# Optimization experiments

Hardware: AMD Instinct MI355X
Metric: run time of the kernel (lower is better)

The kernel has to match this reference:

```python
import jax, jax.numpy as jnp
import numpy as np

N_ENT = 2000
GAT_EMB = 64
GAT_HID = 3
HIDDEN = 256
BATCH = 8
ALPHA = 0.2  # LeakyReLU negative slope
MASK_FILL = jnp.float32(9e-15)  # original fills masked-out logits with 9e-15 (NOT -inf)


def setup_inputs() -> dict:
    key = jax.random.key(0)
    k1, k2, k3, k4, k5, k6 = jax.random.split(key, 6)
    emb = jax.random.normal(k1, (N_ENT, GAT_EMB), dtype=jnp.float32)
    W = jax.random.normal(k2, (GAT_EMB, GAT_HID), dtype=jnp.float32) * 0.2
    a = jax.random.normal(k3, (2 * GAT_HID, 1), dtype=jnp.float32) * 0.2
    fc1_w = jax.random.normal(k4, (HIDDEN, N_ENT * GAT_HID), dtype=jnp.float32) * 0.02
    fc1_b = jax.random.normal(k5, (HIDDEN,), dtype=jnp.float32) * 0.02
    adj = jax.random.randint(k6, (BATCH, N_ENT, N_ENT), 0, 2, dtype=jnp.int32)
    return {"emb": emb, "W": W, "a": a, "fc1_w": fc1_w, "fc1_b": fc1_b, "adj": adj}


def reference(emb, W, a, fc1_w, fc1_b, adj):
    # h = emb @ W : [N, 3] -- shared across all graphs in the batch
    h = emb @ W
    # Pairwise logits: original concatenates [h_i, h_j] and dots with a;
    # equivalent to (h @ a1)_i + (h @ a2)_j via broadcasting (no O(N^2*2H) tensor).
    s1 = h @ a[:GAT_HID, 0]   # [N]
    s2 = h @ a[GAT_HID:, 0]   # [N]
    e = jax.nn.leaky_relu(s1[:, None] + s2[None, :], negative_slope=ALPHA)  # [N, N]
    # Mask by adjacency (fill 9e-15, matching original), softmax over neighbors (dim=1)
    masked = jnp.where(adj > 0, e[None, :, :], MASK_FILL)  # [B, N, N]
    att = jax.nn.softmax(masked, axis=2)
    # Weighted aggregation + ELU (concat=True head)
    h_prime = jnp.einsum('bij,jd->bid', att, h)  # [B, N, 3]
    x = jax.nn.elu(h_prime).reshape(att.shape[0], -1)  # [B, N*3]
    return x @ fc1_w.T + fc1_b  # [B, hidden]
```

## Files before the change

### kernel.cpp

```cpp
#include <hip/hip_runtime.h>
#include <cstddef>

#define N_ENT   2000
#define GAT_EMB 64
#define GAT_HID 3
#define HIDDEN  256
#define BATCH   8
#define ALPHA   0.2f

#define WS_S1_F   8192
#define WS_BYTES  40960

__global__ __launch_bounds__(256) void k_init(const float* __restrict__ fc1_b,
                                              float* __restrict__ out) {
    int idx = blockIdx.x * 256 + threadIdx.x;
    out[idx] = fc1_b[idx & (HIDDEN - 1)];
}

__global__ __launch_bounds__(256) void k_prep(const float* __restrict__ emb,
                                              const float* __restrict__ W,
                                              const float* __restrict__ a,
                                              float* __restrict__ ws) {
    __shared__ float sW[GAT_EMB * GAT_HID];
    __shared__ float sa[2 * GAT_HID];
    int t = threadIdx.x;
    if (t < GAT_EMB * GAT_HID) sW[t] = W[t];
    if (t < 2 * GAT_HID)       sa[t] = a[t];
    __syncthreads();
    int i = blockIdx.x * 256 + t;
    if (i >= N_ENT) return;
    const float4* er = (const float4*)(emb + (size_t)i * GAT_EMB);
    float h0 = 0.f, h1 = 0.f, h2 = 0.f;
#pragma unroll
    for (int k4 = 0; k4 < GAT_EMB / 4; ++k4) {
        float4 e4 = er[k4];
        int k = 4 * k4;
        h0 += e4.x * sW[(k + 0) * 3 + 0]; h1 += e4.x * sW[(k + 0) * 3 + 1]; h2 += e4.x * sW[(k + 0) * 3 + 2];
        h0 += e4.y * sW[(k + 1) * 3 + 0]; h1 += e4.y * sW[(k + 1) * 3 + 1]; h2 += e4.y * sW[(k + 1) * 3 + 2];
        h0 += e4.z * sW[(k + 2) * 3 + 0]; h1 += e4.z * sW[(k + 2) * 3 + 1]; h2 += e4.z * sW[(k + 2) * 3 + 2];
        h0 += e4.w * sW[(k + 3) * 3 + 0]; h1 += e4.w * sW[(k + 3) * 3 + 1]; h2 += e4.w * sW[(k + 3) * 3 + 2];
    }
    ((float4*)ws)[i] = make_float4(h0 * sa[3] + h1 * sa[4] + h2 * sa[5], h0, h1, h2);
    ws[WS_S1_F + i] = h0 * sa[0] + h1 * sa[1] + h2 * sa[2];
}

__global__ __launch_bounds__(256) void k_main(const float* __restrict__ emb,
                                              const float* __restrict__ W,
                                              const float* __restrict__ a,
                                              const float* __restrict__ fc1_w,
                                              const int*   __restrict__ adj,
                                              const float* __restrict__ wsrc,
                                              int use_ws,
                                              float* __restrict__ out) {
    __shared__ float4 spack[N_ENT];
    __shared__ float  sW[GAT_EMB * GAT_HID];
    __shared__ float  sa[2 * GAT_HID];
    __shared__ float  s1_own[2];
    __shared__ float  xblk[BATCH][8];

    int t  = threadIdx.x;
    int i0 = blockIdx.x * 2;

    if (use_ws) {
        const float4* src = (const float4*)wsrc;
        for (int j = t; j < N_ENT; j += 256) spack[j] = src[j];
        if (t < 2) s1_own[t] = wsrc[WS_S1_F + i0 + t];
    } else {
        if (t < GAT_EMB * GAT_HID) sW[t] = W[t];
        if (t < 2 * GAT_HID)       sa[t] = a[t];
        __syncthreads();
        for (int j = t; j < N_ENT; j += 256) {
            const float4* er = (const float4*)(emb + (size_t)j * GAT_EMB);
            float h0 = 0.f, h1 = 0.f, h2 = 0.f;
#pragma unroll
            for (int k4 = 0; k4 < GAT_EMB / 4; ++k4) {
                float4 e4 = er[k4];
                int k = 4 * k4;
                h0 += e4.x * sW[(k + 0) * 3 + 0]; h1 += e4.x * sW[(k + 0) * 3 + 1]; h2 += e4.x * sW[(k + 0) * 3 + 2];
                h0 += e4.y * sW[(k + 1) * 3 + 0]; h1 += e4.y * sW[(k + 1) * 3 + 1]; h2 += e4.y * sW[(k + 1) * 3 + 2];
                h0 += e4.z * sW[(k + 2) * 3 + 0]; h1 += e4.z * sW[(k + 2) * 3 + 1]; h2 += e4.z * sW[(k + 2) * 3 + 2];
                h0 += e4.w * sW[(k + 3) * 3 + 0]; h1 += e4.w * sW[(k + 3) * 3 + 1]; h2 += e4.w * sW[(k + 3) * 3 + 2];
            }
            spack[j] = make_float4(h0 * sa[3] + h1 * sa[4] + h2 * sa[5], h0, h1, h2);
            if (j == i0 || j == i0 + 1)
                s1_own[j - i0] = h0 * sa[0] + h1 * sa[1] + h2 * sa[2];
        }
    }
    __syncthreads();

    int lane = t & 63;
    int w    = t >> 6;
    int di   = w >> 1;
    int b0   = (w & 1) * 4;
    int i    = i0 + di;
    float s1v = s1_own[di];
    const int* __restrict__ r0 = adj + ((size_t)(b0 + 0) * N_ENT + i) * N_ENT;
    const int* __restrict__ r1 = adj + ((size_t)(b0 + 1) * N_ENT + i) * N_ENT;
    const int* __restrict__ r2 = adj + ((size_t)(b0 + 2) * N_ENT + i) * N_ENT;
    const int* __restrict__ r3 = adj + ((size_t)(b0 + 3) * N_ENT + i) * N_ENT;

    float as0 = 0.f, x0 = 0.f, y0 = 0.f, z0 = 0.f;
    float as1 = 0.f, x1 = 0.f, y1 = 0.f, z1 = 0.f;
    float as2 = 0.f, x2 = 0.f, y2 = 0.f, z2 = 0.f;
    float as3 = 0.f, x3 = 0.f, y3 = 0.f, z3 = 0.f;

#pragma unroll 2
    for (int k = 0; k < (N_ENT + 63) / 64; ++k) {
        int j = lane + 64 * k;
        if (j < N_ENT) {
            int m0 = r0[j], m1 = r1[j], m2 = r2[j], m3 = r3[j];
            float4 p = spack[j];
            float e  = s1v + p.x;
            float lr = fmaxf(e, 0.f) + ALPHA * fminf(e, 0.f);
            float ev = __expf(lr);
            float e0 = (m0 > 0) ? ev : 1.0f;
            float e1 = (m1 > 0) ? ev : 1.0f;
            float e2 = (m2 > 0) ? ev : 1.0f;
            float e3 = (m3 > 0) ? ev : 1.0f;
            as0 += e0; x0 += e0 * p.y; y0 += e0 * p.z; z0 += e0 * p.w;
            as1 += e1; x1 += e1 * p.y; y1 += e1 * p.z; z1 += e1 * p.w;
            as2 += e2; x2 += e2 * p.y; y2 += e2 * p.z; z2 += e2 * p.w;
            as3 += e3; x3 += e3 * p.y; y3 += e3 * p.z; z3 += e3 * p.w;
        }
    }
#pragma unroll
    for (int off = 32; off > 0; off >>= 1) {
        as0 += __shfl_xor(as0, off, 64); x0 += __shfl_xor(x0, off, 64);
        y0  += __shfl_xor(y0,  off, 64); z0 += __shfl_xor(z0, off, 64);
        as1 += __shfl_xor(as1, off, 64); x1 += __shfl_xor(x1, off, 64);
        y1  += __shfl_xor(y1,  off, 64); z1 += __shfl_xor(z1, off, 64);
        as2 += __shfl_xor(as2, off, 64); x2 += __shfl_xor(x2, off, 64);
        y2  += __shfl_xor(y2,  off, 64); z2 += __shfl_xor(z2, off, 64);
        as3 += __shfl_xor(as3, off, 64); x3 += __shfl_xor(x3, off, 64);
        y3  += __shfl_xor(y3,  off, 64); z3 += __shfl_xor(z3, off, 64);
    }
    if (lane == 0) {
        float inv, p0, p1, p2;
        inv = 1.f / as0; p0 = x0 * inv; p1 = y0 * inv; p2 = z0 * inv;
        xblk[b0+0][3*di+0] = (p0 > 0.f) ? p0 : expm1f(p0);
        xblk[b0+0][3*di+1] = (p1 > 0.f) ? p1 : expm1f(p1);
        xblk[b0+0][3*di+2] = (p2 > 0.f) ? p2 : expm1f(p2);
        inv = 1.f / as1; p0 = x1 * inv; p1 = y1 * inv; p2 = z1 * inv;
        xblk[b0+1][3*di+0] = (p0 > 0.f) ? p0 : expm1f(p0);
        xblk[b0+1][3*di+1] = (p1 > 0.f) ? p1 : expm1f(p1);
        xblk[b0+1][3*di+2] = (p2 > 0.f) ? p2 : expm1f(p2);
        inv = 1.f / as2; p0 = x2 * inv; p1 = y2 * inv; p2 = z2 * inv;
        xblk[b0+2][3*di+0] = (p0 > 0.f) ? p0 : expm1f(p0);
        xblk[b0+2][3*di+1] = (p1 > 0.f) ? p1 : expm1f(p1);
        xblk[b0+2][3*di+2] = (p2 > 0.f) ? p2 : expm1f(p2);
        inv = 1.f / as3; p0 = x3 * inv; p1 = y3 * inv; p2 = z3 * inv;
        xblk[b0+3][3*di+0] = (p0 > 0.f) ? p0 : expm1f(p0);
        xblk[b0+3][3*di+1] = (p1 > 0.f) ? p1 : expm1f(p1);
        xblk[b0+3][3*di+2] = (p2 > 0.f) ? p2 : expm1f(p2);
    }
    __syncthreads();

    {
        int k = t;
        const float2* wr2 = (const float2*)(fc1_w + (size_t)k * (N_ENT * GAT_HID) + 3 * i0);
        float2 w01 = wr2[0], w23 = wr2[1], w45 = wr2[2];
#pragma unroll
        for (int b = 0; b < BATCH; ++b) {
            float d = xblk[b][0] * w01.x + xblk[b][1] * w01.y
                    + xblk[b][2] * w23.x + xblk[b][3] * w23.y
                    + xblk[b][4] * w45.x + xblk[b][5] * w45.y;
            atomicAdd(&out[b * HIDDEN + k], d);
        }
    }
}

extern "C" void kernel_launch(void* const* d_in, const int* in_sizes, int n_in,
                              void* d_out, int out_size, void* d_ws, size_t ws_size,
                              hipStream_t stream) {
    const float* emb   = (const float*)d_in[0];
    const float* W     = (const float*)d_in[1];
    const float* a     = (const float*)d_in[2];
    const float* fc1_w = (const float*)d_in[3];
    const float* fc1_b = (const float*)d_in[4];
    const int*   adj   = (const int*)d_in[5];
    float* out = (float*)d_out;
    float* ws  = (float*)d_ws;

    int use_ws = (ws_size >= (size_t)WS_BYTES) ? 1 : 0;
    k_init<<<8, 256, 0, stream>>>(fc1_b, out);
    if (use_ws) k_prep<<<8, 256, 0, stream>>>(emb, W, a, ws);
    k_main<<<N_ENT / 2, 256, 0, stream>>>(emb, W, a, fc1_w, adj, ws, use_ws, out);
}
```

Before: 242.6 us.

## Process four rows per block with int4 adjacency loads and SoA shared layout

Each block now handles four rows (one per wavefront) and each wavefront covers all eight batches, loading adjacency as int4 vectors so every lane consumes four columns per iteration. The packed float4 shared array is split into separate s2/h0/h1/h2 arrays for vectorized shared reads, and the workspace layout changes to match. Each exp is now reused across eight batches instead of four, and there are half as many blocks and atomics. In exchange each thread holds a 32-float accumulator array plus eight int4 masks, which raises register pressure and may lower occupancy on this memory-bound adjacency stream.

Result: faster. 218.0 us (-10.1%).

```diff
diff --git a/kernel.cpp b/kernel.cpp
--- a/kernel.cpp
+++ b/kernel.cpp
@@ -2,13 +2,13 @@
 #include <cstddef>
 
 #define N_ENT   2000
+#define NPAD    2048
 #define GAT_EMB 64
 #define GAT_HID 3
 #define HIDDEN  256
 #define BATCH   8
 #define ALPHA   0.2f
 
-#define WS_S1_F   8192
 #define WS_BYTES  40960
 
 __global__ __launch_bounds__(256) void k_init(const float* __restrict__ fc1_b,
@@ -40,8 +40,11 @@
         h0 += e4.z * sW[(k + 2) * 3 + 0]; h1 += e4.z * sW[(k + 2) * 3 + 1]; h2 += e4.z * sW[(k + 2) * 3 + 2];
         h0 += e4.w * sW[(k + 3) * 3 + 0]; h1 += e4.w * sW[(k + 3) * 3 + 1]; h2 += e4.w * sW[(k + 3) * 3 + 2];
     }
-    ((float4*)ws)[i] = make_float4(h0 * sa[3] + h1 * sa[4] + h2 * sa[5], h0, h1, h2);
-    ws[WS_S1_F + i] = h0 * sa[0] + h1 * sa[1] + h2 * sa[2];
+    ws[0 * NPAD + i] = h0 * sa[3] + h1 * sa[4] + h2 * sa[5];
+    ws[1 * NPAD + i] = h0;
+    ws[2 * NPAD + i] = h1;
+    ws[3 * NPAD + i] = h2;
+    ws[4 * NPAD + i] = h0 * sa[0] + h1 * sa[1] + h2 * sa[2];
 }
 
 __global__ __launch_bounds__(256) void k_main(const float* __restrict__ emb,
@@ -52,19 +55,27 @@
                                               const float* __restrict__ wsrc,
                                               int use_ws,
                                               float* __restrict__ out) {
-    __shared__ float4 spack[N_ENT];
-    __shared__ float  sW[GAT_EMB * GAT_HID];
-    __shared__ float  sa[2 * GAT_HID];
-    __shared__ float  s1_own[2];
-    __shared__ float  xblk[BATCH][8];
+    __shared__ __align__(16) float s2s[NPAD];
+    __shared__ __align__(16) float h0s[NPAD];
+    __shared__ __align__(16) float h1s[NPAD];
+    __shared__ __align__(16) float h2s[NPAD];
+    __shared__ float sW[GAT_EMB * GAT_HID];
+    __shared__ float sa[2 * GAT_HID];
+    __shared__ float s1_own[4];
+    __shared__ float xblk[BATCH][16];
 
     int t  = threadIdx.x;
-    int i0 = blockIdx.x * 2;
+    int i0 = blockIdx.x * 4;
 
     if (use_ws) {
-        const float4* src = (const float4*)wsrc;
-        for (int j = t; j < N_ENT; j += 256) spack[j] = src[j];
-        if (t < 2) s1_own[t] = wsrc[WS_S1_F + i0 + t];
+        const float4* s = (const float4*)wsrc;
+        for (int idx = t; idx < N_ENT / 4; idx += 256) {
+            ((float4*)s2s)[idx] = s[0 * (NPAD / 4) + idx];
+            ((float4*)h0s)[idx] = s[1 * (NPAD / 4) + idx];
+            ((float4*)h1s)[idx] = s[2 * (NPAD / 4) + idx];
+            ((float4*)h2s)[idx] = s[3 * (NPAD / 4) + idx];
+        }
+        if (t < 4) s1_own[t] = wsrc[4 * NPAD + i0 + t];
     } else {
         if (t < GAT_EMB * GAT_HID) sW[t] = W[t];
         if (t < 2 * GAT_HID)       sa[t] = a[t];
@@ -81,8 +92,9 @@
                 h0 += e4.z * sW[(k + 2) * 3 + 0]; h1 += e4.z * sW[(k + 2) * 3 + 1]; h2 += e4.z * sW[(k + 2) * 3 + 2];
                 h0 += e4.w * sW[(k + 3) * 3 + 0]; h1 += e4.w * sW[(k + 3) * 3 + 1]; h2 += e4.w * sW[(k + 3) * 3 + 2];
             }
-            spack[j] = make_float4(h0 * sa[3] + h1 * sa[4] + h2 * sa[5], h0, h1, h2);
-            if (j == i0 || j == i0 + 1)
+            s2s[j] = h0 * sa[3] + h1 * sa[4] + h2 * sa[5];
+            h0s[j] = h0; h1s[j] = h1; h2s[j] = h2;
+            if (j >= i0 && j < i0 + 4)
                 s1_own[j - i0] = h0 * sa[0] + h1 * sa[1] + h2 * sa[2];
         }
     }
@@ -90,80 +102,79 @@
 
     int lane = t & 63;
     int w    = t >> 6;
-    int di   = w >> 1;
-    int b0   = (w & 1) * 4;
-    int i    = i0 + di;
-    float s1v = s1_own[di];
-    const int* __restrict__ r0 = adj + ((size_t)(b0 + 0) * N_ENT + i) * N_ENT;
-    const int* __restrict__ r1 = adj + ((size_t)(b0 + 1) * N_ENT + i) * N_ENT;
-    const int* __restrict__ r2 = adj + ((size_t)(b0 + 2) * N_ENT + i) * N_ENT;
-    const int* __restrict__ r3 = adj + ((size_t)(b0 + 3) * N_ENT + i) * N_ENT;
+    int i    = i0 + w;
+    float s1v = s1_own[w];
+    const int* __restrict__ base = adj + (size_t)i * N_ENT;
 
-    float as0 = 0.f, x0 = 0.f, y0 = 0.f, z0 = 0.f;
-    float as1 = 0.f, x1 = 0.f, y1 = 0.f, z1 = 0.f;
-    float as2 = 0.f, x2 = 0.f, y2 = 0.f, z2 = 0.f;
-    float as3 = 0.f, x3 = 0.f, y3 = 0.f, z3 = 0.f;
+    float acc[BATCH][4];
+#pragma unroll
+    for (int b = 0; b < BATCH; ++b) { acc[b][0] = 0.f; acc[b][1] = 0.f; acc[b][2] = 0.f; acc[b][3] = 0.f; }
 
-#pragma unroll 2
-    for (int k = 0; k < (N_ENT + 63) / 64; ++k) {
-        int j = lane + 64 * k;
-        if (j < N_ENT) {
-            int m0 = r0[j], m1 = r1[j], m2 = r2[j], m3 = r3[j];
-            float4 p = spack[j];
-            float e  = s1v + p.x;
-            float lr = fmaxf(e, 0.f) + ALPHA * fminf(e, 0.f);
-            float ev = __expf(lr);
-            float e0 = (m0 > 0) ? ev : 1.0f;
-            float e1 = (m1 > 0) ? ev : 1.0f;
-            float e2 = (m2 > 0) ? ev : 1.0f;
-            float e3 = (m3 > 0) ? ev : 1.0f;
-            as0 += e0; x0 += e0 * p.y; y0 += e0 * p.z; z0 += e0 * p.w;
-            as1 += e1; x1 += e1 * p.y; y1 += e1 * p.z; z1 += e1 * p.w;
-            as2 += e2; x2 += e2 * p.y; y2 += e2 * p.z; z2 += e2 * p.w;
-            as3 += e3; x3 += e3 * p.y; y3 += e3 * p.z; z3 += e3 * p.w;
+#pragma unroll 1
+    for (int k = 0; k < (N_ENT + 255) / 256; ++k) {
+        int j0 = k * 256 + lane * 4;
+        if (j0 < N_ENT) {
+            int4 m[BATCH];
+#pragma unroll
+            for (int b = 0; b < BATCH; ++b)
+                m[b] = *(const int4*)(base + (size_t)b * (N_ENT * N_ENT) + j0);
+            float4 s2v = *(const float4*)&s2s[j0];
+            float4 h0v = *(const float4*)&h0s[j0];
+            float4 h1v = *(const float4*)&h1s[j0];
+            float4 h2v = *(const float4*)&h2s[j0];
+            float ev[4];
+#pragma unroll
+            for (int q = 0; q < 4; ++q) {
+                float e  = s1v + ((const float*)&s2v)[q];
+                float lr = fmaxf(e, 0.f) + ALPHA * fminf(e, 0.f);
+                ev[q] = __expf(lr);
+            }
+#pragma unroll
+            for (int b = 0; b < BATCH; ++b) {
+                const int* mb = (const int*)&m[b];
+#pragma unroll
+                for (int q = 0; q < 4; ++q) {
+                    float e = (mb[q] > 0) ? ev[q] : 1.0f;
+                    acc[b][0] += e;
+                    acc[b][1] += e * ((const float*)&h0v)[q];
+                    acc[b][2] += e * ((const float*)&h1v)[q];
+                    acc[b][3] += e * ((const float*)&h2v)[q];
+                }
+            }
         }
     }
+
 #pragma unroll
-    for (int off = 32; off > 0; off >>= 1) {
-        as0 += __shfl_xor(as0, off, 64); x0 += __shfl_xor(x0, off, 64);
-        y0  += __shfl_xor(y0,  off, 64); z0 += __shfl_xor(z0, off, 64);
-        as1 += __shfl_xor(as1, off, 64); x1 += __shfl_xor(x1, off, 64);
-        y1  += __shfl_xor(y1,  off, 64); z1 += __shfl_xor(z1, off, 64);
-        as2 += __shfl_xor(as2, off, 64); x2 += __shfl_xor(x2, off, 64);
-        y2  += __shfl_xor(y2,  off, 64); z2 += __shfl_xor(z2, off, 64);
-        as3 += __shfl_xor(as3, off, 64); x3 += __shfl_xor(x3, off, 64);
-        y3  += __shfl_xor(y3,  off, 64); z3 += __shfl_xor(z3, off, 64);
-    }
+    for (int off = 32; off > 0; off >>= 1)
+#pragma unroll
+        for (int b = 0; b < BATCH; ++b) {
+            acc[b][0] += __shfl_xor(acc[b][0], off, 64);
+            acc[b][1] += __shfl_xor(acc[b][1], off, 64);
+            acc[b][2] += __shfl_xor(acc[b][2], off, 64);
+            acc[b][3] += __shfl_xor(acc[b][3], off, 64);
+        }
+
     if (lane == 0) {
-        float inv, p0, p1, p2;
-        inv = 1.f / as0; p0 = x0 * inv; p1 = y0 * inv; p2 = z0 * inv;
-        xblk[b0+0][3*di+0] = (p0 > 0.f) ? p0 : expm1f(p0);
-        xblk[b0+0][3*di+1] = (p1 > 0.f) ? p1 : expm1f(p1);
-        xblk[b0+0][3*di+2] = (p2 > 0.f) ? p2 : expm1f(p2);
-        inv = 1.f / as1; p0 = x1 * inv; p1 = y1 * inv; p2 = z1 * inv;
-        xblk[b0+1][3*di+0] = (p0 > 0.f) ? p0 : expm1f(p0);
-        xblk[b0+1][3*di+1] = (p1 > 0.f) ? p1 : expm1f(p1);
-        xblk[b0+1][3*di+2] = (p2 > 0.f) ? p2 : expm1f(p2);
-        inv = 1.f / as2; p0 = x2 * inv; p1 = y2 * inv; p2 = z2 * inv;
-        xblk[b0+2][3*di+0] = (p0 > 0.f) ? p0 : expm1f(p0);
-        xblk[b0+2][3*di+1] = (p1 > 0.f) ? p1 : expm1f(p1);
-        xblk[b0+2][3*di+2] = (p2 > 0.f) ? p2 : expm1f(p2);
-        inv = 1.f / as3; p0 = x3 * inv; p1 = y3 * inv; p2 = z3 * inv;
-        xblk[b0+3][3*di+0] = (p0 > 0.f) ? p0 : expm1f(p0);
-        xblk[b0+3][3*di+1] = (p1 > 0.f) ? p1 : expm1f(p1);
-        xblk[b0+3][3*di+2] = (p2 > 0.f) ? p2 : expm1f(p2);
+#pragma unroll
+        for (int b = 0; b < BATCH; ++b) {
+            float inv = 1.f / acc[b][0];
+            float p0 = acc[b][1] * inv, p1 = acc[b][2] * inv, p2 = acc[b][3] * inv;
+            xblk[b][3 * w + 0] = (p0 > 0.f) ? p0 : expm1f(p0);
+            xblk[b][3 * w + 1] = (p1 > 0.f) ? p1 : expm1f(p1);
+            xblk[b][3 * w + 2] = (p2 > 0.f) ? p2 : expm1f(p2);
+        }
     }
     __syncthreads();
 
     {
         int k = t;
-        const float2* wr2 = (const float2*)(fc1_w + (size_t)k * (N_ENT * GAT_HID) + 3 * i0);
-        float2 w01 = wr2[0], w23 = wr2[1], w45 = wr2[2];
+        const float4* wr4 = (const float4*)(fc1_w + (size_t)k * (N_ENT * GAT_HID) + 3 * i0);
+        float4 wa = wr4[0], wb = wr4[1], wc = wr4[2];
 #pragma unroll
         for (int b = 0; b < BATCH; ++b) {
-            float d = xblk[b][0] * w01.x + xblk[b][1] * w01.y
-                    + xblk[b][2] * w23.x + xblk[b][3] * w23.y
-                    + xblk[b][4] * w45.x + xblk[b][5] * w45.y;
+            float d = xblk[b][0]  * wa.x + xblk[b][1]  * wa.y + xblk[b][2]  * wa.z + xblk[b][3]  * wa.w
+                    + xblk[b][4]  * wb.x + xblk[b][5]  * wb.y + xblk[b][6]  * wb.z + xblk[b][7]  * wb.w
+                    + xblk[b][8]  * wc.x + xblk[b][9]  * wc.y + xblk[b][10] * wc.z + xblk[b][11] * wc.w;
             atomicAdd(&out[b * HIDDEN + k], d);
         }
     }
@@ -184,5 +195,5 @@
     int use_ws = (ws_size >= (size_t)WS_BYTES) ? 1 : 0;
     k_init<<<8, 256, 0, stream>>>(fc1_b, out);
     if (use_ws) k_prep<<<8, 256, 0, stream>>>(emb, W, a, ws);
-    k_main<<<N_ENT / 2, 256, 0, stream>>>(emb, W, a, fc1_w, adj, ws, use_ws, out);
+    k_main<<<N_ENT / 4, 256, 0, stream>>>(emb, W, a, fc1_w, adj, ws, use_ws, out);
 }
```
